# Kernel optimization log

Measured on AMD Instinct MI355X. Metric: run time of the kernel, lower is better.

## Reference

```python
import jax, jax.numpy as jnp
import numpy as np

B, T, C = 4, 2048, 1024
H, Dh = 16, 64
EPS = 1e-5

def _layernorm(x, g, b):
    mu = jnp.mean(x, axis=-1, keepdims=True)
    var = jnp.mean(jnp.square(x - mu), axis=-1, keepdims=True)
    return (x - mu) * jax.lax.rsqrt(var + EPS) * g + b

def setup_inputs() -> dict:
    key = jax.random.key(0)
    ks = jax.random.split(key, 12)
    s = lambda fan_in: 1.0 / np.sqrt(fan_in)
    return {
        "x":  jax.random.normal(ks[0], (B, T, C), dtype=jnp.float32),
        "Wq": jax.random.uniform(ks[1], (C, H * Dh), jnp.float32, -s(C), s(C)),
        "Wk": jax.random.uniform(ks[2], (C, H * Dh), jnp.float32, -s(C), s(C)),
        "Wv": jax.random.uniform(ks[3], (C, H * Dh), jnp.float32, -s(C), s(C)),
        "Wo": jax.random.uniform(ks[4], (H * Dh, C), jnp.float32, -s(H * Dh), s(H * Dh)),
        "bo": jnp.zeros((C,), jnp.float32),
        "W1": jax.random.uniform(ks[5], (C, 4 * C), jnp.float32, -s(C), s(C)),
        "b1": jnp.zeros((4 * C,), jnp.float32),
        "W2": jax.random.uniform(ks[6], (4 * C, C), jnp.float32, -s(4 * C), s(4 * C)),
        "b2": jnp.zeros((C,), jnp.float32),
        "g1": jnp.ones((C,), jnp.float32),
        "be1": jnp.zeros((C,), jnp.float32),
        "g2": jnp.ones((C,), jnp.float32),
        "be2": jnp.zeros((C,), jnp.float32),
    }

def reference(x, Wq, Wk, Wv, Wo, bo, W1, b1, W2, b2, g1, be1, g2, be2):
    # --- pre-LN attention ---
    h = _layernorm(x, g1, be1)                                   # [B,T,C]
    q = (h @ Wq).reshape(B, T, H, Dh)                            # per-head projections fused
    k = (h @ Wk).reshape(B, T, H, Dh)
    v = (h @ Wv).reshape(B, T, H, Dh)
    scores = jnp.einsum('bqhd,bkhd->bhqk', q, k) * (Dh ** -0.5)  # [B,H,T,T]
    causal = jnp.tril(jnp.ones((T, T), dtype=bool))
    scores = jnp.where(causal, scores, -jnp.inf)
    wei = jax.nn.softmax(scores, axis=-1)                        # dropout p=0 (eval)
    attn = jnp.einsum('bhqk,bkhd->bqhd', wei, v).reshape(B, T, H * Dh)
    x = x + attn @ Wo + bo
    # --- pre-LN MLP ---
    h2 = _layernorm(x, g2, be2)
    x = x + jax.nn.relu(h2 @ W1 + b1) @ W2 + b2
    return x
```

## Files before the change

kernel.cpp:

```cpp
#include <hip/hip_runtime.h>
#include <hip/hip_bf16.h>

typedef __hip_bfloat16 bf16;
typedef __attribute__((ext_vector_type(8))) short short8;
typedef __attribute__((ext_vector_type(4))) short s16x4;
typedef __attribute__((ext_vector_type(4))) float f32x4;

__device__ __forceinline__ float s2f(short s) {
    unsigned u = ((unsigned)(unsigned short)s) << 16;
    return __builtin_bit_cast(float, u);
}
__device__ __forceinline__ short f2s(float f) {
    bf16 h = __float2bfloat16(f);
    return __builtin_bit_cast(short, h);
}
__device__ __forceinline__ void gload_lds16(const void* g, void* l) {
    __builtin_amdgcn_global_load_lds(
        (const __attribute__((address_space(1))) unsigned int*)g,
        (__attribute__((address_space(3))) unsigned int*)l, 16, 0, 0);
}

#define PH_VM8  asm volatile("s_waitcnt vmcnt(8)" ::: "memory")
#define PH_VM4  asm volatile("s_waitcnt vmcnt(4)" ::: "memory")
#define PH_VM0  asm volatile("s_waitcnt vmcnt(0)" ::: "memory")
#define PH_BAR  __builtin_amdgcn_s_barrier()
#define PH_LGKM do { asm volatile("s_waitcnt lgkmcnt(0)" ::: "memory"); \
                     __builtin_amdgcn_sched_barrier(0); } while (0)

__global__ __launch_bounds__(256) void tconv_kernel(const float* __restrict__ src,
                                                    short* __restrict__ dst,
                                                    int R, int C) {
    __shared__ short tile[64][65];
    const int r0 = blockIdx.y * 64, c0 = blockIdx.x * 64;
    const int t = threadIdx.x;
    const int lr = t >> 2, lc = (t & 3) * 16;
    const float* sp = src + (size_t)(r0 + lr) * C + c0 + lc;
#pragma unroll
    for (int q = 0; q < 4; q++) {
        f32x4 v = *(const f32x4*)(const void*)(sp + q * 4);
#pragma unroll
        for (int j = 0; j < 4; j++) tile[lr][lc + q * 4 + j] = f2s(v[j]);
    }
    __syncthreads();
    short8 o0, o1;
#pragma unroll
    for (int j = 0; j < 8; j++) { o0[j] = tile[lc + j][lr]; o1[j] = tile[lc + 8 + j][lr]; }
    short* dp = dst + (size_t)(c0 + lr) * R + r0 + lc;
    *(short8*)(void*)dp = o0;
    *(short8*)(void*)(dp + 8) = o1;
}

__global__ __launch_bounds__(256) void ln_kernel(const float* __restrict__ x,
                                                 const float* __restrict__ g,
                                                 const float* __restrict__ beta,
                                                 bf16* __restrict__ out) {
    const int t = threadIdx.x;
    const int w = t >> 6, lane = t & 63;
    const int row = blockIdx.x * 4 + w;
    const float* xr = x + (size_t)row * 1024;
    float v[16];
    float s = 0.f, ss = 0.f;
#pragma unroll
    for (int p = 0; p < 4; p++) {
        f32x4 xv = *(const f32x4*)(const void*)(xr + p * 256 + lane * 4);
#pragma unroll
        for (int j = 0; j < 4; j++) {
            v[p * 4 + j] = xv[j];
            s += xv[j];
            ss += xv[j] * xv[j];
        }
    }
#pragma unroll
    for (int off = 32; off >= 1; off >>= 1) {
        s += __shfl_xor(s, off);
        ss += __shfl_xor(ss, off);
    }
    const float mu = s * (1.0f / 1024.0f);
    const float var = ss * (1.0f / 1024.0f) - mu * mu;
    const float rstd = rsqrtf(var + 1e-5f);
    short* orow = (short*)(void*)(out + (size_t)row * 1024);
#pragma unroll
    for (int p = 0; p < 4; p++) {
        const int c = p * 256 + lane * 4;
        f32x4 gv = *(const f32x4*)(const void*)(g + c);
        f32x4 bv = *(const f32x4*)(const void*)(beta + c);
        s16x4 o;
#pragma unroll
        for (int j = 0; j < 4; j++)
            o[j] = f2s((v[p * 4 + j] - mu) * rstd * gv[j] + bv[j]);
        *(s16x4*)(void*)(orow + c) = o;
    }
}

__global__ __launch_bounds__(256) void gemm64(const bf16* __restrict__ A,
                                              const bf16* __restrict__ Bt,
                                              const float* __restrict__ bias,
                                              const float* resid,
                                              void* Cp, int c_f32,
                                              int m_base, int N, int K,
                                              int relu_flag) {
    __shared__ short As[64 * 64];
    __shared__ short Bs[64 * 64];

    const int t = threadIdx.x;
    const int m0 = blockIdx.x * 64;
    const int n0 = blockIdx.y * 64;
    const int w = t >> 6;
    const int lane = t & 63;
    const int wm = (w >> 1) * 32;
    const int wn = (w & 1) * 32;

    const int sr = t >> 2, sk = (t & 3) * 8;
    const bf16* aA = A + (size_t)(m0 + sr) * K + sk;
    const bf16* aB = Bt + (size_t)(n0 + sr) * K + sk;
    short* ldsA0 = &As[w * 512];
    short* ldsA1 = &As[2048 + w * 512];
    short* ldsB0 = &Bs[w * 512];
    short* ldsB1 = &Bs[2048 + w * 512];

    const int l = lane & 15;
    const int lk = (lane >> 4) * 8;

    f32x4 acc[2][2] = {};

    for (int k0 = 0; k0 < K; k0 += 64) {
        __syncthreads();
        gload_lds16(aA + k0, ldsA0);
        gload_lds16(aA + k0 + 32, ldsA1);
        gload_lds16(aB + k0, ldsB0);
        gload_lds16(aB + k0 + 32, ldsB1);
        __syncthreads();
#pragma unroll
        for (int ks = 0; ks < 2; ks++) {
            short8 a0 = *(const short8*)&As[ks * 2048 + (wm + l) * 32 + lk];
            short8 a1 = *(const short8*)&As[ks * 2048 + (wm + 16 + l) * 32 + lk];
            short8 b0 = *(const short8*)&Bs[ks * 2048 + (wn + l) * 32 + lk];
            short8 b1 = *(const short8*)&Bs[ks * 2048 + (wn + 16 + l) * 32 + lk];
            acc[0][0] = __builtin_amdgcn_mfma_f32_16x16x32_bf16(a0, b0, acc[0][0], 0, 0, 0);
            acc[0][1] = __builtin_amdgcn_mfma_f32_16x16x32_bf16(a0, b1, acc[0][1], 0, 0, 0);
            acc[1][0] = __builtin_amdgcn_mfma_f32_16x16x32_bf16(a1, b0, acc[1][0], 0, 0, 0);
            acc[1][1] = __builtin_amdgcn_mfma_f32_16x16x32_bf16(a1, b1, acc[1][1], 0, 0, 0);
        }
    }

    const int lrow4 = (lane >> 4) * 4;
#pragma unroll
    for (int mi = 0; mi < 2; mi++)
#pragma unroll
        for (int r = 0; r < 4; r++) {
            const int grow = m_base + m0 + wm + mi * 16 + lrow4 + r;
#pragma unroll
            for (int ni = 0; ni < 2; ni++) {
                const int gcol = n0 + wn + ni * 16 + l;
                float val = acc[mi][ni][r];
                if (bias) val += bias[gcol];
                if (relu_flag) val = fmaxf(val, 0.f);
                const size_t ci = (size_t)grow * N + gcol;
                if (resid) val += resid[ci];
                if (c_f32) ((float*)Cp)[ci] = val;
                else        ((short*)Cp)[ci] = f2s(val);
            }
        }
}

#define MM_BLOCK(ACC)                                                        \
    do {                                                                     \
        __builtin_amdgcn_s_setprio(1);                                       \
        _Pragma("unroll")                                                    \
        for (int mi_ = 0; mi_ < 4; mi_++)                                    \
            _Pragma("unroll")                                                \
            for (int ni_ = 0; ni_ < 4; ni_++)                                \
                ACC[mi_][ni_] = __builtin_amdgcn_mfma_f32_16x16x32_bf16(     \
                    af[mi_], bf[ni_], ACC[mi_][ni_], 0, 0, 0);               \
        __builtin_amdgcn_s_setprio(0);                                       \
    } while (0)

__global__ __launch_bounds__(512, 2) void gemm256(const bf16* __restrict__ A,
                                                  const bf16* __restrict__ Bt,
                                                  const float* __restrict__ bias,
                                                  bf16* __restrict__ Cp,
                                                  int N, int relu_flag) {
    __shared__ char lds[131072];
    constexpr int NT = 16;

    const int t = threadIdx.x;
    const int w = t >> 6, lane = t & 63;
    const int l = lane & 15, g = lane >> 4;
    const int m0 = blockIdx.x * 256, n0 = blockIdx.y * 256;
    const int wm = (w >> 2) * 128, wn = (w & 3) * 64;
    const int qx = (g ^ ((l >> 1) & 3)) * 16;
    const int qh8 = (((lane & 3) ^ ((lane >> 3) & 3)) * 8);
    const int srow = w * 32 + (lane >> 2);
    const short* Asrc = (const short*)A;
    const short* Bsrc = (const short*)Bt;

    f32x4 accL[4][4] = {};
    f32x4 accH[4][4] = {};
    short8 af[4], bf[4];

    auto stage = [&](int th, int j) {
        const int ks = j >> 1, mat = j & 1;
        char* slot = lds + ((th & 1) << 16) + (mat << 15) + (ks << 14);
        const short* mp = mat ? Bsrc : Asrc;
        const int rowb = (mat ? n0 : m0);
        const int kc = th * 64 + ks * 32 + qh8;
        gload_lds16(mp + (size_t)(rowb + srow) * 1024 + kc,      slot + (w * 2) * 1024);
        gload_lds16(mp + (size_t)(rowb + srow + 16) * 1024 + kc, slot + (w * 2 + 1) * 1024);
    };
    auto lda = [&](const char* rb, int mi, int ks) -> short8 {
        return *(const short8*)(rb + (ks << 14) + (wm + mi * 16 + l) * 64 + qx);
    };
    auto ldb = [&](const char* rb, int ni, int ks) -> short8 {
        return *(const short8*)(rb + 32768 + (ks << 14) + (wn + ni * 16 + l) * 64 + qx);
    };

    stage(0, 0); stage(0, 1); stage(0, 2); stage(0, 3); stage(1, 0); stage(1, 1);

    for (int it = 0; it < NT - 1; ++it) {
        const char* rb = lds + ((it & 1) << 16);
        PH_VM8; PH_BAR;
#pragma unroll
        for (int i = 0; i < 4; i++) af[i] = lda(rb, i, 0);
#pragma unroll
        for (int i = 0; i < 4; i++) bf[i] = ldb(rb, i, 0);
        stage(it + 1, 2);
        PH_LGKM;
        MM_BLOCK(accL);
#pragma unroll
        for (int i = 0; i < 4; i++) af[i] = lda(rb, 4 + i, 0);
        stage(it + 1, 3);
        PH_BAR; PH_LGKM;
        MM_BLOCK(accH);
        PH_VM8; PH_BAR;
#pragma unroll
        for (int i = 0; i < 4; i++) af[i] = lda(rb, i, 1);
#pragma unroll
        for (int i = 0; i < 4; i++) bf[i] = ldb(rb, i, 1);
        if (it + 2 < NT) stage(it + 2, 0);
        PH_LGKM;
        MM_BLOCK(accL);
#pragma unroll
        for (int i = 0; i < 4; i++) af[i] = lda(rb, 4 + i, 1);
        if (it + 2 < NT) stage(it + 2, 1);
        PH_BAR; PH_LGKM;
        MM_BLOCK(accH);
    }
    {
        const char* rb = lds + (((NT - 1) & 1) << 16);
        PH_VM4; PH_BAR;
#pragma unroll
        for (int i = 0; i < 4; i++) af[i] = lda(rb, i, 0);
#pragma unroll
        for (int i = 0; i < 4; i++) bf[i] = ldb(rb, i, 0);
        PH_LGKM;
        MM_BLOCK(accL);
#pragma unroll
        for (int i = 0; i < 4; i++) af[i] = lda(rb, 4 + i, 0);
        PH_BAR; PH_LGKM;
        MM_BLOCK(accH);
        PH_VM0; PH_BAR;
#pragma unroll
        for (int i = 0; i < 4; i++) af[i] = lda(rb, i, 1);
#pragma unroll
        for (int i = 0; i < 4; i++) bf[i] = ldb(rb, i, 1);
        PH_LGKM;
        MM_BLOCK(accL);
#pragma unroll
        for (int i = 0; i < 4; i++) af[i] = lda(rb, 4 + i, 1);
        PH_BAR; PH_LGKM;
        MM_BLOCK(accH);
    }

#pragma unroll
    for (int half = 0; half < 2; half++)
#pragma unroll
        for (int mi = 0; mi < 4; mi++)
#pragma unroll
            for (int r = 0; r < 4; r++) {
                const int grow = m0 + wm + (half * 4 + mi) * 16 + g * 4 + r;
                short* crow = (short*)(void*)Cp + (size_t)grow * N;
#pragma unroll
                for (int ni = 0; ni < 4; ni++) {
                    const int gcol = n0 + wn + ni * 16 + l;
                    float val = half ? accH[mi][ni][r] : accL[mi][ni][r];
                    if (bias) val += bias[gcol];
                    if (relu_flag) val = fmaxf(val, 0.f);
                    crow[gcol] = f2s(val);
                }
            }
}

__global__ __launch_bounds__(256) void attn_kernel(const bf16* __restrict__ qkv,
                                                   bf16* __restrict__ o) {
    __shared__ short KsF[2][4096];
    __shared__ short Vt[64][72];
    __shared__ short Pl[4][32][76];

    const int bh = blockIdx.x;
    const int b = bh >> 4, h = bh & 15;
    const int qt = 15 - blockIdx.y;
    const int q0 = qt * 128;
    const size_t rbase = (size_t)b * 2048;
    const int hcol = h * 64;

    const int t = threadIdx.x;
    const int w = t >> 6;
    const int lane = t & 63;
    const int l = lane & 15;
    const int g = lane >> 4;
    const int sp = t >> 3;
    const int sb = (t & 7) * 8;

    const int qw0 = q0 + 32 * w;
    short8 qf[2][2];
#pragma unroll
    for (int mi = 0; mi < 2; mi++)
#pragma unroll
        for (int ks = 0; ks < 2; ks++) {
            const short* qp = (const short*)qkv +
                (rbase + qw0 + mi * 16 + l) * 3072 + hcol + ks * 32 + g * 8;
            short8 tv = *(const short8*)(const void*)qp;
            short8 sv;
#pragma unroll
            for (int e = 0; e < 8; e++) sv[e] = f2s(s2f(tv[e]) * 0.125f);
            qf[mi][ks] = sv;
        }

    const int key_a = w * 16 + (lane >> 3);
    const int kd = (lane & 7) ^ ((lane >> 3) & 7);
    const short* kgA = (const short*)qkv + (rbase + key_a) * 3072 + 1024 + hcol + kd * 8;
    const short* kgB = kgA + 8 * 3072;

    f32x4 o_acc[2][4] = {};
    float l_sum[2] = {0.f, 0.f};
    const f32x4 s_init = {-12.f, -12.f, -12.f, -12.f};

    const int kt_max = (q0 + 127) >> 6;

    gload_lds16(kgA, &KsF[0][w * 1024]);
    gload_lds16(kgB, &KsF[0][w * 1024 + 512]);

    for (int kt = 0; kt <= kt_max; kt++) {
        const int k0 = kt * 64;
        const short* vg = (const short*)qkv + (rbase + k0 + 2 * sp) * 3072 + 2048 + hcol + sb;
        short8 vv0 = *(const short8*)(const void*)vg;
        short8 vv1 = *(const short8*)(const void*)(vg + 3072);
        PH_BAR;
        {
            const int kp = (kt < kt_max) ? (kt + 1) : kt;
            const size_t kof = (size_t)kp * 64 * 3072;
            gload_lds16(kgA + kof, &KsF[(kt + 1) & 1][w * 1024]);
            gload_lds16(kgB + kof, &KsF[(kt + 1) & 1][w * 1024 + 512]);
        }
        asm volatile("s_waitcnt vmcnt(2)" ::: "memory");
        __builtin_amdgcn_sched_barrier(0);
        {
            const int key = 2 * sp;
            const int cbk = key >> 3;
            const int kin = key & 7;
#pragma unroll
            for (int j = 0; j < 8; j++) {
                const int d = sb + j;
                const int col = ((cbk ^ (d >> 3)) << 3) + kin;
                int pk = (int)(unsigned short)vv0[j] | ((int)(unsigned short)vv1[j] << 16);
                *(int*)(void*)&Vt[d][col] = pk;
            }
        }
        asm volatile("s_waitcnt lgkmcnt(0)" ::: "memory");
        __builtin_amdgcn_sched_barrier(0);
        PH_BAR;

        if (k0 <= qw0 + 31) {
            const short* kb = &KsF[kt & 1][0];
            const bool needMask = (k0 + 63 > qw0);
            f32x4 s_acc[2][4];
#pragma unroll
            for (int mi = 0; mi < 2; mi++)
#pragma unroll
                for (int ni = 0; ni < 4; ni++) s_acc[mi][ni] = s_init;
#pragma unroll
            for (int ks = 0; ks < 2; ks++) {
                short8 kf[4];
#pragma unroll
                for (int ni = 0; ni < 4; ni++) {
                    const int key = ni * 16 + l;
                    const int c = key * 8 + ((ks * 4 + g) ^ (key & 7));
                    kf[ni] = *(const short8*)&kb[c * 8];
                }
#pragma unroll
                for (int mi = 0; mi < 2; mi++)
#pragma unroll
                    for (int ni = 0; ni < 4; ni++)
                        s_acc[mi][ni] = __builtin_amdgcn_mfma_f32_16x16x32_bf16(
                            kf[ni], qf[mi][ks], s_acc[mi][ni], 0, 0, 0);
            }
#pragma unroll
            for (int mi = 0; mi < 2; mi++) {
                const int qg = qw0 + mi * 16 + l;
#pragma unroll
                for (int ni = 0; ni < 4; ni++) {
                    const int keyb = k0 + ni * 16 + 4 * g;
                    s16x4 pv;
#pragma unroll
                    for (int r = 0; r < 4; r++) {
                        float s = s_acc[mi][ni][r];
                        if (needMask && (keyb + r > qg)) s = -1e30f;
                        const float pe = __expf(s);
                        l_sum[mi] += pe;
                        pv[r] = f2s(pe);
                    }
                    *(s16x4*)(void*)&Pl[w][mi * 16 + l][ni * 16 + 4 * g] = pv;
                }
            }
#pragma unroll
            for (int ks = 0; ks < 2; ks++) {
                short8 pf[2], vf[4];
#pragma unroll
                for (int mi = 0; mi < 2; mi++)
                    pf[mi] = *(const short8*)&Pl[w][mi * 16 + l][ks * 32 + g * 8];
#pragma unroll
                for (int nd = 0; nd < 4; nd++) {
                    const int d = nd * 16 + l;
                    const int cb = ks * 4 + g;
                    vf[nd] = *(const short8*)&Vt[d][((cb ^ (d >> 3)) << 3)];
                }
#pragma unroll
                for (int mi = 0; mi < 2; mi++)
#pragma unroll
                    for (int nd = 0; nd < 4; nd++)
                        o_acc[mi][nd] = __builtin_amdgcn_mfma_f32_16x16x32_bf16(
                            pf[mi], vf[nd], o_acc[mi][nd], 0, 0, 0);
            }
        }
    }

#pragma unroll
    for (int mi = 0; mi < 2; mi++) {
        l_sum[mi] += __shfl_xor(l_sum[mi], 16);
        l_sum[mi] += __shfl_xor(l_sum[mi], 32);
    }

#pragma unroll
    for (int mi = 0; mi < 2; mi++)
#pragma unroll
        for (int r = 0; r < 4; r++) {
            const float lsum = __shfl(l_sum[mi], 4 * g + r);
            const float inv = 1.0f / lsum;
            const int qg = qw0 + mi * 16 + 4 * g + r;
            short* op = (short*)(void*)(o + (rbase + qg) * 1024 + hcol);
#pragma unroll
            for (int nd = 0; nd < 4; nd++)
                op[nd * 16 + l] = f2s(o_acc[mi][nd][r] * inv);
        }
}

extern "C" void kernel_launch(void* const* d_in, const int* in_sizes, int n_in,
                              void* d_out, int out_size, void* d_ws, size_t ws_size,
                              hipStream_t stream) {
    const float* x   = (const float*)d_in[0];
    const float* Wq  = (const float*)d_in[1];
    const float* Wk  = (const float*)d_in[2];
    const float* Wv  = (const float*)d_in[3];
    const float* Wo  = (const float*)d_in[4];
    const float* bo  = (const float*)d_in[5];
    const float* W1  = (const float*)d_in[6];
    const float* b1  = (const float*)d_in[7];
    const float* W2  = (const float*)d_in[8];
    const float* b2  = (const float*)d_in[9];
    const float* g1  = (const float*)d_in[10];
    const float* be1 = (const float*)d_in[11];
    const float* g2  = (const float*)d_in[12];
    const float* be2 = (const float*)d_in[13];

    char* ws = (char*)d_ws;
    const size_t MB = (size_t)1024 * 1024;
    bf16*  s0  = (bf16*)(ws);
    bf16*  qkv = (bf16*)(ws + 16 * MB);
    short* WoT = (short*)(ws + 16 * MB);
    short* W1T = (short*)(ws);
    short* W2T = (short*)(ws + 8 * MB);
    bf16*  h2  = (bf16*)(ws + 16 * MB);
    bf16*  m1  = (bf16*)(ws + 32 * MB);
    short* WT  = (short*)d_out;
    float* x1  = (float*)d_out;

    const int M = 8192, C = 1024, F = 4096, MH = 4096;

    tconv_kernel<<<dim3(16, 16), 256, 0, stream>>>(Wq, WT,                   C, C);
    tconv_kernel<<<dim3(16, 16), 256, 0, stream>>>(Wk, WT + 1024 * 1024,     C, C);
    tconv_kernel<<<dim3(16, 16), 256, 0, stream>>>(Wv, WT + 2 * 1024 * 1024, C, C);

    ln_kernel<<<M / 4, 256, 0, stream>>>(x, g1, be1, s0);

    gemm256<<<dim3(M / 256, 3072 / 256), 512, 0, stream>>>(
        s0, (const bf16*)WT, nullptr, qkv, 3072, 0);

    attn_kernel<<<dim3(64, 16), 256, 0, stream>>>(qkv, s0);

    tconv_kernel<<<dim3(16, 16), 256, 0, stream>>>(Wo, WoT, C, C);
    gemm64<<<dim3(M / 64, C / 64), 256, 0, stream>>>(
        s0, (const bf16*)WoT, bo, x, x1, 1, 0, C, C, 0);

    tconv_kernel<<<dim3(64, 16), 256, 0, stream>>>(W1, W1T, C, F);
    tconv_kernel<<<dim3(16, 64), 256, 0, stream>>>(W2, W2T, F, C);

    ln_kernel<<<M / 4, 256, 0, stream>>>(x1, g2, be2, h2);

    for (int half = 0; half < 2; half++) {
        const bf16* Ah = h2 + (size_t)half * MH * C;
        gemm256<<<dim3(MH / 256, F / 256), 512, 0, stream>>>(
            Ah, (const bf16*)W1T, b1, m1, F, 1);
        gemm64<<<dim3(MH / 64, C / 64), 256, 0, stream>>>(
            m1, (const bf16*)W2T, b2, x1, d_out, 1, half * MH, C, F, 0);
    }
}
```

Measured before the change: 566.4 us.

## Replace 64x64 residual GEMM with pipelined 128x128 double-buffered swizzled GEMM

Swaps the simple 64x64-tile gemm64 kernel, which synchronizes around every k-step, for a 128x128-tile kernel. The new kernel double-buffers LDS, issues global-to-LDS loads one or two k-tiles ahead with vmcnt-based waits, uses an XOR-swizzled LDS layout to avoid bank conflicts, and interleaves MFMA blocks with the loads. It is meant to cut global traffic per FLOP and hide load latency in the Wo and W2 projections, which include bias and residual. In exchange it uses 64KB of LDS and more accumulators, and at N=1024 it launches fewer blocks (512 for Wo, 256 per W2 half).

New measurement: 553.2 us. 1.02x faster.

```diff
diff --git a/kernel.cpp b/kernel.cpp
--- a/kernel.cpp
+++ b/kernel.cpp
@@ -92,75 +92,128 @@
     }
 }
 
-__global__ __launch_bounds__(256) void gemm64(const bf16* __restrict__ A,
-                                              const bf16* __restrict__ Bt,
-                                              const float* __restrict__ bias,
-                                              const float* resid,
-                                              void* Cp, int c_f32,
-                                              int m_base, int N, int K,
-                                              int relu_flag) {
-    __shared__ short As[64 * 64];
-    __shared__ short Bs[64 * 64];
+#define MM_BLK2(ACC)                                                         \
+    do {                                                                     \
+        __builtin_amdgcn_s_setprio(1);                                       \
+        _Pragma("unroll")                                                    \
+        for (int mi_ = 0; mi_ < 2; mi_++)                                    \
+            _Pragma("unroll")                                                \
+            for (int ni_ = 0; ni_ < 4; ni_++)                                \
+                ACC[mi_][ni_] = __builtin_amdgcn_mfma_f32_16x16x32_bf16(     \
+                    af[mi_], bf[ni_], ACC[mi_][ni_], 0, 0, 0);               \
+        __builtin_amdgcn_s_setprio(0);                                       \
+    } while (0)
+
+__global__ __launch_bounds__(256, 2) void gemm128(const bf16* __restrict__ A,
+                                                  const bf16* __restrict__ Bt,
+                                                  const float* __restrict__ bias,
+                                                  const float* resid,
+                                                  void* Cp, int c_f32,
+                                                  int m_base, int N, int K,
+                                                  int relu_flag) {
+    __shared__ char lds[65536];
+    const int NT = K >> 6;
 
     const int t = threadIdx.x;
-    const int m0 = blockIdx.x * 64;
-    const int n0 = blockIdx.y * 64;
-    const int w = t >> 6;
-    const int lane = t & 63;
-    const int wm = (w >> 1) * 32;
-    const int wn = (w & 1) * 32;
-
-    const int sr = t >> 2, sk = (t & 3) * 8;
-    const bf16* aA = A + (size_t)(m0 + sr) * K + sk;
-    const bf16* aB = Bt + (size_t)(n0 + sr) * K + sk;
-    short* ldsA0 = &As[w * 512];
-    short* ldsA1 = &As[2048 + w * 512];
-    short* ldsB0 = &Bs[w * 512];
-    short* ldsB1 = &Bs[2048 + w * 512];
-
-    const int l = lane & 15;
-    const int lk = (lane >> 4) * 8;
-
-    f32x4 acc[2][2] = {};
-
-    for (int k0 = 0; k0 < K; k0 += 64) {
-        __syncthreads();
-        gload_lds16(aA + k0, ldsA0);
-        gload_lds16(aA + k0 + 32, ldsA1);
-        gload_lds16(aB + k0, ldsB0);
-        gload_lds16(aB + k0 + 32, ldsB1);
-        __syncthreads();
-#pragma unroll
-        for (int ks = 0; ks < 2; ks++) {
-            short8 a0 = *(const short8*)&As[ks * 2048 + (wm + l) * 32 + lk];
-            short8 a1 = *(const short8*)&As[ks * 2048 + (wm + 16 + l) * 32 + lk];
-            short8 b0 = *(const short8*)&Bs[ks * 2048 + (wn + l) * 32 + lk];
-            short8 b1 = *(const short8*)&Bs[ks * 2048 + (wn + 16 + l) * 32 + lk];
-            acc[0][0] = __builtin_amdgcn_mfma_f32_16x16x32_bf16(a0, b0, acc[0][0], 0, 0, 0);
-            acc[0][1] = __builtin_amdgcn_mfma_f32_16x16x32_bf16(a0, b1, acc[0][1], 0, 0, 0);
-            acc[1][0] = __builtin_amdgcn_mfma_f32_16x16x32_bf16(a1, b0, acc[1][0], 0, 0, 0);
-            acc[1][1] = __builtin_amdgcn_mfma_f32_16x16x32_bf16(a1, b1, acc[1][1], 0, 0, 0);
-        }
-    }
-
-    const int lrow4 = (lane >> 4) * 4;
-#pragma unroll
-    for (int mi = 0; mi < 2; mi++)
-#pragma unroll
-        for (int r = 0; r < 4; r++) {
-            const int grow = m_base + m0 + wm + mi * 16 + lrow4 + r;
-#pragma unroll
-            for (int ni = 0; ni < 2; ni++) {
-                const int gcol = n0 + wn + ni * 16 + l;
-                float val = acc[mi][ni][r];
-                if (bias) val += bias[gcol];
-                if (relu_flag) val = fmaxf(val, 0.f);
-                const size_t ci = (size_t)grow * N + gcol;
-                if (resid) val += resid[ci];
-                if (c_f32) ((float*)Cp)[ci] = val;
-                else        ((short*)Cp)[ci] = f2s(val);
+    const int w = t >> 6, lane = t & 63;
+    const int l = lane & 15, g = lane >> 4;
+    const int m0 = blockIdx.x * 128, n0 = blockIdx.y * 128;
+    const int wm = (w >> 1) * 64, wn = (w & 1) * 64;
+    const int qx = (g ^ ((l >> 1) & 3)) * 16;
+    const int qh8 = (((lane & 3) ^ ((lane >> 3) & 3)) * 8);
+    const int srow = w * 32 + (lane >> 2);
+    const short* Asrc = (const short*)A;
+    const short* Bsrc = (const short*)Bt;
+
+    f32x4 accL[2][4] = {};
+    f32x4 accH[2][4] = {};
+    short8 af[2], bf[4];
+
+    auto stage = [&](int th, int j) {
+        const int ks = j >> 1, mat = j & 1;
+        char* slot = lds + ((th & 1) << 15) + (mat << 14) + (ks << 13);
+        const short* mp = mat ? Bsrc : Asrc;
+        const int rowb = (mat ? n0 : m0);
+        const int kc = th * 64 + ks * 32 + qh8;
+        gload_lds16(mp + (size_t)(rowb + srow) * K + kc,      slot + w * 2048);
+        gload_lds16(mp + (size_t)(rowb + srow + 16) * K + kc, slot + w * 2048 + 1024);
+    };
+    auto lda_ = [&](const char* rb, int mi, int ks) -> short8 {
+        return *(const short8*)(rb + (ks << 13) + (wm + mi * 16 + l) * 64 + qx);
+    };
+    auto ldb_ = [&](const char* rb, int ni, int ks) -> short8 {
+        return *(const short8*)(rb + 16384 + (ks << 13) + (wn + ni * 16 + l) * 64 + qx);
+    };
+
+    stage(0, 0); stage(0, 1); stage(0, 2); stage(0, 3); stage(1, 0); stage(1, 1);
+
+    for (int it = 0; it < NT - 1; ++it) {
+        const char* rb = lds + ((it & 1) << 15);
+        PH_VM8; PH_BAR;
+        af[0] = lda_(rb, 0, 0); af[1] = lda_(rb, 1, 0);
+#pragma unroll
+        for (int i = 0; i < 4; i++) bf[i] = ldb_(rb, i, 0);
+        stage(it + 1, 2);
+        PH_LGKM;
+        MM_BLK2(accL);
+        af[0] = lda_(rb, 2, 0); af[1] = lda_(rb, 3, 0);
+        stage(it + 1, 3);
+        PH_BAR; PH_LGKM;
+        MM_BLK2(accH);
+        PH_VM8; PH_BAR;
+        af[0] = lda_(rb, 0, 1); af[1] = lda_(rb, 1, 1);
+#pragma unroll
+        for (int i = 0; i < 4; i++) bf[i] = ldb_(rb, i, 1);
+        if (it + 2 < NT) stage(it + 2, 0);
+        PH_LGKM;
+        MM_BLK2(accL);
+        af[0] = lda_(rb, 2, 1); af[1] = lda_(rb, 3, 1);
+        if (it + 2 < NT) stage(it + 2, 1);
+        PH_BAR; PH_LGKM;
+        MM_BLK2(accH);
+    }
+    {
+        const char* rb = lds + (((NT - 1) & 1) << 15);
+        PH_VM4; PH_BAR;
+        af[0] = lda_(rb, 0, 0); af[1] = lda_(rb, 1, 0);
+#pragma unroll
+        for (int i = 0; i < 4; i++) bf[i] = ldb_(rb, i, 0);
+        PH_LGKM;
+        MM_BLK2(accL);
+        af[0] = lda_(rb, 2, 0); af[1] = lda_(rb, 3, 0);
+        PH_BAR; PH_LGKM;
+        MM_BLK2(accH);
+        PH_VM0; PH_BAR;
+        af[0] = lda_(rb, 0, 1); af[1] = lda_(rb, 1, 1);
+#pragma unroll
+        for (int i = 0; i < 4; i++) bf[i] = ldb_(rb, i, 1);
+        PH_LGKM;
+        MM_BLK2(accL);
+        af[0] = lda_(rb, 2, 1); af[1] = lda_(rb, 3, 1);
+        PH_BAR; PH_LGKM;
+        MM_BLK2(accH);
+    }
+
+#pragma unroll
+    for (int half = 0; half < 2; half++)
+#pragma unroll
+        for (int mi = 0; mi < 2; mi++)
+#pragma unroll
+            for (int r = 0; r < 4; r++) {
+                const int grow = m_base + m0 + wm + (half * 2 + mi) * 16 + g * 4 + r;
+                const size_t rowoff = (size_t)grow * N;
+#pragma unroll
+                for (int ni = 0; ni < 4; ni++) {
+                    const int gcol = n0 + wn + ni * 16 + l;
+                    float val = half ? accH[mi][ni][r] : accL[mi][ni][r];
+                    if (bias) val += bias[gcol];
+                    if (relu_flag) val = fmaxf(val, 0.f);
+                    const size_t ci = rowoff + gcol;
+                    if (resid) val += resid[ci];
+                    if (c_f32) ((float*)Cp)[ci] = val;
+                    else       ((short*)Cp)[ci] = f2s(val);
+                }
             }
-        }
 }
 
 #define MM_BLOCK(ACC)                                                        \
@@ -498,7 +551,7 @@
     attn_kernel<<<dim3(64, 16), 256, 0, stream>>>(qkv, s0);
 
     tconv_kernel<<<dim3(16, 16), 256, 0, stream>>>(Wo, WoT, C, C);
-    gemm64<<<dim3(M / 64, C / 64), 256, 0, stream>>>(
+    gemm128<<<dim3(M / 128, C / 128), 256, 0, stream>>>(
         s0, (const bf16*)WoT, bo, x, x1, 1, 0, C, C, 0);
 
     tconv_kernel<<<dim3(64, 16), 256, 0, stream>>>(W1, W1T, C, F);
@@ -510,7 +563,7 @@
         const bf16* Ah = h2 + (size_t)half * MH * C;
         gemm256<<<dim3(MH / 256, F / 256), 512, 0, stream>>>(
             Ah, (const bf16*)W1T, b1, m1, F, 1);
-        gemm64<<<dim3(MH / 64, C / 64), 256, 0, stream>>>(
+        gemm128<<<dim3(MH / 128, C / 128), 256, 0, stream>>>(
             m1, (const bf16*)W2T, b2, x1, d_out, 1, half * MH, C, F, 0);
     }
 }
```
